# Kernel optimization log

Measured on AMD Instinct MI355X. Metric: run time of the kernel, lower is better.

## Reference

```python
import jax, jax.numpy as jnp
import numpy as np

L, H, P = 16384, 1024, 512
DT_MIN, DT_MAX = 1e-3, 1e-1


def setup_inputs() -> dict:
    key = jax.random.key(0)
    ks = jax.random.split(key, 9)
    input_sequence = jax.random.normal(ks[0], (L, H), dtype=jnp.float32)
    # HiPPO-like diagonal init: negative real parts, spread imaginary parts
    Lambda_re = -0.5 * jnp.ones((P,), dtype=jnp.float32)
    Lambda_im = jnp.pi * jnp.arange(P, dtype=jnp.float32)
    # B_tilde = Vinv @ B with lecun_normal B -> ~N(0, 1/H) entries
    B_re = jax.random.normal(ks[1], (P, H), dtype=jnp.float32) / np.float32(np.sqrt(H))
    B_im = jax.random.normal(ks[2], (P, H), dtype=jnp.float32) / np.float32(np.sqrt(H))
    # C_tilde = C @ V, lecun_normal scale ~1/sqrt(2P)
    C_re = jax.random.normal(ks[3], (H, P), dtype=jnp.float32) / np.float32(np.sqrt(2 * P))
    C_im = jax.random.normal(ks[4], (H, P), dtype=jnp.float32) / np.float32(np.sqrt(2 * P))
    D = jax.random.normal(ks[5], (H,), dtype=jnp.float32)
    # log_step ~ U[log(dt_min), log(dt_max)], shape (P, 1)
    u01 = jax.random.uniform(ks[6], (P, 1), dtype=jnp.float32)
    log_step = jnp.log(DT_MIN) + u01 * (jnp.log(DT_MAX) - jnp.log(DT_MIN))
    return {
        "input_sequence": input_sequence,
        "Lambda_re": Lambda_re, "Lambda_im": Lambda_im,
        "B_re": B_re, "B_im": B_im,
        "C_re": C_re, "C_im": C_im,
        "D": D, "log_step": log_step,
    }


def _binop(q_i, q_j):
    # diagonal linear recurrence combine: x_j = A_j * x_i + b_j
    A_i, b_i = q_i
    A_j, b_j = q_j
    return (A_j * A_i, A_j * b_i + b_j)


def reference(input_sequence, Lambda_re, Lambda_im, B_re, B_im, C_re, C_im, D, log_step):
    # step_rescale = 1.0, clip_eigs = False, conj_sym = True, zoh discretization
    step = jnp.exp(log_step[:, 0])                      # (P,)
    Lam = Lambda_re + 1j * Lambda_im                    # (P,) complex64
    Lambda_bar = jnp.exp(Lam * step)                    # (P,)
    B_tilde = B_re + 1j * B_im                          # (P, H)
    B_bar = ((Lambda_bar - 1.0) / Lam)[:, None] * B_tilde  # (P, H)

    # bf16-split complex matvec: Bu_t = B_bar @ u_t (u real) for all t at once
    Bre_bf = jnp.real(B_bar).astype(jnp.bfloat16)
    Bim_bf = jnp.imag(B_bar).astype(jnp.bfloat16)
    u_bf = input_sequence.astype(jnp.bfloat16)          # (L, H)
    Bu_re = jnp.einsum('ph,lh->lp', Bre_bf, u_bf).astype(jnp.float32)
    Bu_im = jnp.einsum('ph,lh->lp', Bim_bf, u_bf).astype(jnp.float32)
    Bu = Bu_re + 1j * Bu_im                             # (L, P) complex64

    Lambda_elems = Lambda_bar * jnp.ones((input_sequence.shape[0], Lambda_bar.shape[0]),
                                         dtype=Lambda_bar.dtype)  # (L, P)
    _, xs = jax.lax.associative_scan(_binop, (Lambda_elems, Bu))  # xs: (L, P) complex64

    # bf16-split complex matvec y = C_tilde @ x, keep real part only
    Cre_bf = C_re.astype(jnp.bfloat16)
    Cim_bf = C_im.astype(jnp.bfloat16)
    xre_bf = jnp.real(xs).astype(jnp.bfloat16)
    xim_bf = jnp.imag(xs).astype(jnp.bfloat16)
    rr = jnp.einsum('hp,lp->lh', Cre_bf, xre_bf)
    ii = jnp.einsum('hp,lp->lh', Cim_bf, xim_bf)
    y_real = (rr - ii).astype(jnp.float32)              # (L, H)
    ys = 2.0 * y_real                                   # conj_sym doubling

    # feedthrough
    return ys + D * input_sequence
```

## Files before the change

### kernel.cpp

```cpp
#include <hip/hip_runtime.h>
#include <stdint.h>
#include <stddef.h>

#define L_SEQ 16384
#define H_DIM 1024
#define P_DIM 512
#define N2P   1024
#define CHUNK 64
#define NCH   256

#define NB_U 8192
#define NB_B 256
#define NB_C 512
#define NB_T 2

typedef __bf16 bf16x8 __attribute__((ext_vector_type(8)));
typedef float  f32x4  __attribute__((ext_vector_type(4)));
typedef unsigned short u16x8 __attribute__((ext_vector_type(8)));
typedef unsigned int   u32x4 __attribute__((ext_vector_type(4)));

__device__ __forceinline__ unsigned short f2bf(float x) {
  unsigned int u = __float_as_uint(x);
  u += 0x7FFFu + ((u >> 16) & 1u);
  return (unsigned short)(u >> 16);
}
__device__ __forceinline__ float bf2f(unsigned short x) {
  return __uint_as_float((unsigned int)x << 16);
}

__global__ void k_pack_all(const float* __restrict__ U, unsigned short* __restrict__ Ub,
                           const float* __restrict__ Bre, const float* __restrict__ Bim,
                           unsigned short* __restrict__ Bp,
                           const float* __restrict__ Cre, const float* __restrict__ Cim,
                           unsigned short* __restrict__ Cp,
                           const float* __restrict__ Lre, const float* __restrict__ Lim,
                           const float* __restrict__ lstep,
                           float2* __restrict__ lam, float2* __restrict__ lamK) {
  int bid = blockIdx.x, tid = threadIdx.x;
  if (bid < NB_U) {
    size_t base = ((size_t)bid * 256 + tid) * 8;
    const float4* s = (const float4*)(U + base);
    float4 v0 = s[0], v1 = s[1];
    u16x8 o;
    o[0] = f2bf(v0.x); o[1] = f2bf(v0.y); o[2] = f2bf(v0.z); o[3] = f2bf(v0.w);
    o[4] = f2bf(v1.x); o[5] = f2bf(v1.y); o[6] = f2bf(v1.z); o[7] = f2bf(v1.w);
    *(u16x8*)(Ub + base) = o;
  } else if (bid < NB_U + NB_B) {
    int base = ((bid - NB_U) * 256 + tid) * 8;
    int p = base >> 10, h = base & 1023;
    float step = __expf(0.f) , sv, cv;
    step = expf(lstep[p]);
    float ar = Lre[p] * step, ai = Lim[p] * step;
    float er = expf(ar);
    sincosf(ai, &sv, &cv);
    float lr = er * cv, li = er * sv;
    float nr = lr - 1.0f, ni = li;
    float dr = Lre[p], di = Lim[p];
    float den = dr * dr + di * di;
    float cx = (nr * dr + ni * di) / den;
    float cy = (ni * dr - nr * di) / den;
    const float4* sre = (const float4*)(Bre + base);
    const float4* sim = (const float4*)(Bim + base);
    float4 r0 = sre[0], r1 = sre[1], i0 = sim[0], i1 = sim[1];
    u16x8 ore, oim;
    ore[0] = f2bf(cx * r0.x - cy * i0.x);  oim[0] = f2bf(cx * i0.x + cy * r0.x);
    ore[1] = f2bf(cx * r0.y - cy * i0.y);  oim[1] = f2bf(cx * i0.y + cy * r0.y);
    ore[2] = f2bf(cx * r0.z - cy * i0.z);  oim[2] = f2bf(cx * i0.z + cy * r0.z);
    ore[3] = f2bf(cx * r0.w - cy * i0.w);  oim[3] = f2bf(cx * i0.w + cy * r0.w);
    ore[4] = f2bf(cx * r1.x - cy * i1.x);  oim[4] = f2bf(cx * i1.x + cy * r1.x);
    ore[5] = f2bf(cx * r1.y - cy * i1.y);  oim[5] = f2bf(cx * i1.y + cy * r1.y);
    ore[6] = f2bf(cx * r1.z - cy * i1.z);  oim[6] = f2bf(cx * i1.z + cy * r1.z);
    ore[7] = f2bf(cx * r1.w - cy * i1.w);  oim[7] = f2bf(cx * i1.w + cy * r1.w);
    *(u16x8*)(Bp + (size_t)(2 * p) * H_DIM + h)     = ore;
    *(u16x8*)(Bp + (size_t)(2 * p + 1) * H_DIM + h) = oim;
  } else if (bid < NB_U + NB_B + NB_C) {
    int base = ((bid - NB_U - NB_B) * 256 + tid) * 8;
    int h = base >> 10, j0 = base & 1023;
    int p0 = j0 >> 1;
    float4 cr = *(const float4*)(Cre + (size_t)h * P_DIM + p0);
    float4 ci = *(const float4*)(Cim + (size_t)h * P_DIM + p0);
    u16x8 o;
    o[0] = f2bf(cr.x); o[1] = f2bf(-ci.x);
    o[2] = f2bf(cr.y); o[3] = f2bf(-ci.y);
    o[4] = f2bf(cr.z); o[5] = f2bf(-ci.z);
    o[6] = f2bf(cr.w); o[7] = f2bf(-ci.w);
    *(u16x8*)(Cp + base) = o;
  } else {
    int p = (bid - NB_U - NB_B - NB_C) * 256 + tid;
    if (p < P_DIM) {
      double step = exp((double)lstep[p]);
      double ar = (double)Lre[p] * step, ai = (double)Lim[p] * step;
      double er = exp(ar);
      lam[p] = make_float2((float)(er * cos(ai)), (float)(er * sin(ai)));
      double ka = (double)CHUNK * ai, kr = exp((double)CHUNK * ar);
      lamK[p] = make_float2((float)(kr * cos(ka)), (float)(kr * sin(ka)));
    }
  }
}

template <int OUT>
__global__ void gemm_bt(const unsigned short* __restrict__ A,
                        const unsigned short* __restrict__ B,
                        void* __restrict__ Cout,
                        const unsigned short* __restrict__ Ub,
                        const float* __restrict__ Dv) {
  const int K = 1024, N = 1024;
  __shared__ unsigned short sA[128 * 64];
  __shared__ unsigned short sB[128 * 64];
  const int tid = threadIdx.x;
  const int wave = tid >> 6, lane = tid & 63;
  const int quad = lane >> 4, l16 = lane & 15;
  const int m0 = blockIdx.x * 128, n0 = blockIdx.y * 128;
  const int wm = (wave & 1) * 64, wn = (wave >> 1) * 64;

  f32x4 acc[4][4] = {};

  for (int kt = 0; kt < K; kt += 64) {
    __syncthreads();
#pragma unroll
    for (int r = 0; r < 4; ++r) {
      int s = r * 256 + tid;
      int row = s >> 3;
      int j8 = (s & 7) ^ (row & 7);
      const unsigned short* ga = A + (size_t)(m0 + row) * K + kt + j8 * 8;
      const unsigned short* gb = B + (size_t)(n0 + row) * K + kt + j8 * 8;
      __builtin_amdgcn_global_load_lds(
          (const __attribute__((address_space(1))) unsigned int*)ga,
          (__attribute__((address_space(3))) unsigned int*)(sA + (r * 256 + wave * 64) * 8),
          16, 0, 0);
      __builtin_amdgcn_global_load_lds(
          (const __attribute__((address_space(1))) unsigned int*)gb,
          (__attribute__((address_space(3))) unsigned int*)(sB + (r * 256 + wave * 64) * 8),
          16, 0, 0);
    }
    __syncthreads();

#pragma unroll
    for (int h = 0; h < 2; ++h) {
      bf16x8 af[4], bfr[4];
#pragma unroll
      for (int i = 0; i < 4; ++i) {
        int ra = wm + i * 16 + l16;
        af[i] = *(const bf16x8*)(sA + ra * 64 + (((h << 2) + quad) ^ (ra & 7)) * 8);
      }
#pragma unroll
      for (int j = 0; j < 4; ++j) {
        int rb = wn + j * 16 + l16;
        bfr[j] = *(const bf16x8*)(sB + rb * 64 + (((h << 2) + quad) ^ (rb & 7)) * 8);
      }
#pragma unroll
      for (int i = 0; i < 4; ++i)
#pragma unroll
        for (int j = 0; j < 4; ++j)
          acc[i][j] = __builtin_amdgcn_mfma_f32_16x16x32_bf16(af[i], bfr[j], acc[i][j], 0, 0, 0);
    }
  }

#pragma unroll
  for (int i = 0; i < 4; ++i) {
#pragma unroll
    for (int j = 0; j < 4; ++j) {
      int col = n0 + wn + j * 16 + l16;
#pragma unroll
      for (int r = 0; r < 4; ++r) {
        int row = m0 + wm + i * 16 + quad * 4 + r;
        size_t o = (size_t)row * N + col;
        float v = acc[i][j][r];
        if (OUT) {
          float u = bf2f(Ub[o]);
          ((float*)Cout)[o] = 2.0f * v + Dv[col] * u;
        } else {
          ((unsigned short*)Cout)[o] = f2bf(v);
        }
      }
    }
  }
}

__global__ __launch_bounds__(256) void k_scanA(const unsigned short* __restrict__ Bu,
                                               const float2* __restrict__ lam,
                                               float2* __restrict__ csum) {
  __shared__ unsigned int tile[CHUNK * 256];
  const int bid = blockIdx.x;
  const int chunk = bid >> 1, half = bid & 1;
  const int tid = threadIdx.x, wave = tid >> 6, lane = tid & 63;
  const unsigned int* gbase =
      (const unsigned int*)(Bu + (size_t)chunk * CHUNK * N2P) + half * 256;
#pragma unroll
  for (int r = 0; r < 16; ++r) {
    int row = r * 4 + wave;
    __builtin_amdgcn_global_load_lds(
        (const __attribute__((address_space(1))) unsigned int*)
            (gbase + (size_t)row * (N2P / 2) + lane * 4),
        (__attribute__((address_space(3))) unsigned int*)(tile + row * 256),
        16, 0, 0);
  }
  __syncthreads();
  const int p = half * 256 + tid;
  const float2 l = lam[p];
  float xr = 0.f, xi = 0.f;
#pragma unroll 16
  for (int t = 0; t < CHUNK; ++t) {
    unsigned int v = tile[t * 256 + tid];
    float br = bf2f((unsigned short)(v & 0xffffu));
    float bi = bf2f((unsigned short)(v >> 16));
    float nr = fmaf(l.x, xr, fmaf(-l.y, xi, br));
    float ni = fmaf(l.x, xi, fmaf(l.y, xr, bi));
    xr = nr; xi = ni;
  }
  csum[(size_t)chunk * P_DIM + p] = make_float2(xr, xi);
}

__global__ __launch_bounds__(256) void k_scanC(const unsigned short* __restrict__ Bu,
                                               const float2* __restrict__ lam,
                                               const float2* __restrict__ lamK,
                                               const float2* __restrict__ csum,
                                               unsigned short* __restrict__ xs) {
  __shared__ unsigned int tile[CHUNK * 256];
  const int bid = blockIdx.x;
  const int chunk = bid >> 1, half = bid & 1;
  const int tid = threadIdx.x, wave = tid >> 6, lane = tid & 63;
  const unsigned int* gbase =
      (const unsigned int*)(Bu + (size_t)chunk * CHUNK * N2P) + half * 256;
#pragma unroll
  for (int r = 0; r < 16; ++r) {
    int row = r * 4 + wave;
    __builtin_amdgcn_global_load_lds(
        (const __attribute__((address_space(1))) unsigned int*)
            (gbase + (size_t)row * (N2P / 2) + lane * 4),
        (__attribute__((address_space(3))) unsigned int*)(tile + row * 256),
        16, 0, 0);
  }
  const int p = half * 256 + tid;
  const float2 l = lam[p];
  const float2 lk = lamK[p];
  float cr = 0.f, ci = 0.f;
#pragma unroll 4
  for (int j = 0; j < chunk; ++j) {
    float2 s = csum[(size_t)j * P_DIM + p];
    float nr = fmaf(lk.x, cr, fmaf(-lk.y, ci, s.x));
    float ni = fmaf(lk.x, ci, fmaf(lk.y, cr, s.y));
    cr = nr; ci = ni;
  }
  __syncthreads();
  float xr = cr, xi = ci;
#pragma unroll 16
  for (int t = 0; t < CHUNK; ++t) {
    unsigned int v = tile[t * 256 + tid];
    float br = bf2f((unsigned short)(v & 0xffffu));
    float bi = bf2f((unsigned short)(v >> 16));
    float nr = fmaf(l.x, xr, fmaf(-l.y, xi, br));
    float ni = fmaf(l.x, xi, fmaf(l.y, xr, bi));
    xr = nr; xi = ni;
    tile[t * 256 + tid] = (unsigned int)f2bf(xr) | ((unsigned int)f2bf(xi) << 16);
  }
  __syncthreads();
  unsigned int* obase = (unsigned int*)(xs + (size_t)chunk * CHUNK * N2P) + half * 256;
#pragma unroll
  for (int r = 0; r < 16; ++r) {
    int row = r * 4 + wave;
    *(u32x4*)(obase + (size_t)row * (N2P / 2) + lane * 4) =
        *(const u32x4*)(tile + row * 256 + lane * 4);
  }
}

extern "C" void kernel_launch(void* const* d_in, const int* in_sizes, int n_in,
                              void* d_out, int out_size, void* d_ws, size_t ws_size,
                              hipStream_t stream) {
  const float* U    = (const float*)d_in[0];
  const float* Lre  = (const float*)d_in[1];
  const float* Lim  = (const float*)d_in[2];
  const float* Bre  = (const float*)d_in[3];
  const float* Bim  = (const float*)d_in[4];
  const float* Cre  = (const float*)d_in[5];
  const float* Cim  = (const float*)d_in[6];
  const float* Dv   = (const float*)d_in[7];
  const float* lstp = (const float*)d_in[8];
  float* out = (float*)d_out;

  size_t off = 0;
  char* ws = (char*)d_ws;
  auto give = [&](size_t bytes) -> void* {
    void* p = ws + off;
    off += (bytes + 255) & ~(size_t)255;
    return p;
  };

  unsigned short* ubf  = (unsigned short*)give((size_t)L_SEQ * H_DIM * 2);
  unsigned short* Bp   = (unsigned short*)give((size_t)N2P * H_DIM * 2);
  unsigned short* Cp   = (unsigned short*)give((size_t)H_DIM * N2P * 2);
  unsigned short* Bu   = (unsigned short*)give((size_t)L_SEQ * N2P * 2);
  unsigned short* xs   = (unsigned short*)give((size_t)L_SEQ * N2P * 2);
  float2*         lam  = (float2*)give(P_DIM * sizeof(float2));
  float2*         lamK = (float2*)give(P_DIM * sizeof(float2));
  float2*         csum = (float2*)give((size_t)NCH * P_DIM * sizeof(float2));

  k_pack_all<<<NB_U + NB_B + NB_C + NB_T, 256, 0, stream>>>(
      U, ubf, Bre, Bim, Bp, Cre, Cim, Cp, Lre, Lim, lstp, lam, lamK);

  gemm_bt<0><<<dim3(L_SEQ / 128, N2P / 128), 256, 0, stream>>>(ubf, Bp, Bu, nullptr, nullptr);

  k_scanA<<<NCH * 2, 256, 0, stream>>>(Bu, lam, csum);
  k_scanC<<<NCH * 2, 256, 0, stream>>>(Bu, lam, lamK, csum, xs);

  gemm_bt<1><<<dim3(L_SEQ / 128, N2P / 128), 256, 0, stream>>>(xs, Cp, out, ubf, Dv);
}
```

Measured before the change: 262.9 us.

## Enlarge GEMM tiles to 256x256 with double-buffered async LDS loads

Both bf16 GEMMs now use 256x256 output tiles with 512 threads, where each wave computes a 128x64 sub-tile. The global-to-LDS loads are double-buffered: the next K-slice is prefetched while MFMAs run on the current one, with explicit vmcnt waits and barriers, and MFMA sections are raised in priority via s_setprio. This targets load latency and the low data reuse of the 128x128 tiles. The cost is 128KB of LDS per block and higher register use (32 accumulators), which can limit occupancy, and the grid shrinks to 256 blocks.

```diff
diff --git a/kernel.cpp b/kernel.cpp
--- a/kernel.cpp
+++ b/kernel.cpp
@@ -48,8 +48,8 @@
   } else if (bid < NB_U + NB_B) {
     int base = ((bid - NB_U) * 256 + tid) * 8;
     int p = base >> 10, h = base & 1023;
-    float step = __expf(0.f) , sv, cv;
-    step = expf(lstep[p]);
+    float sv, cv;
+    float step = expf(lstep[p]);
     float ar = Lre[p] * step, ai = Lim[p] * step;
     float er = expf(ar);
     sincosf(ai, &sv, &cv);
@@ -99,65 +99,91 @@
 }
 
 template <int OUT>
-__global__ void gemm_bt(const unsigned short* __restrict__ A,
+__global__ __launch_bounds__(512, 2) void gemm_bt(const unsigned short* __restrict__ A,
                         const unsigned short* __restrict__ B,
                         void* __restrict__ Cout,
                         const unsigned short* __restrict__ Ub,
                         const float* __restrict__ Dv) {
   const int K = 1024, N = 1024;
-  __shared__ unsigned short sA[128 * 64];
-  __shared__ unsigned short sB[128 * 64];
+  __shared__ unsigned short sA[2 * 256 * 64];
+  __shared__ unsigned short sB[2 * 256 * 64];
   const int tid = threadIdx.x;
-  const int wave = tid >> 6, lane = tid & 63;
+  const int w = tid >> 6, lane = tid & 63;
   const int quad = lane >> 4, l16 = lane & 15;
-  const int m0 = blockIdx.x * 128, n0 = blockIdx.y * 128;
-  const int wm = (wave & 1) * 64, wn = (wave >> 1) * 64;
-
-  f32x4 acc[4][4] = {};
-
-  for (int kt = 0; kt < K; kt += 64) {
-    __syncthreads();
+  const int m0 = blockIdx.x * 256, n0 = blockIdx.y * 256;
+  const int wm = (w & 1) * 128, wn = (w >> 1) * 64;
+
+  f32x4 acc[8][4] = {};
+
+  const unsigned short* ga[4];
+  const unsigned short* gb[4];
+#pragma unroll
+  for (int r = 0; r < 4; ++r) {
+    int s = r * 512 + tid;
+    int row = s >> 3;
+    int j8 = (s & 7) ^ (row & 7);
+    ga[r] = A + (size_t)(m0 + row) * K + j8 * 8;
+    gb[r] = B + (size_t)(n0 + row) * K + j8 * 8;
+  }
+
+  auto stage = [&](int buf, int kt) {
 #pragma unroll
     for (int r = 0; r < 4; ++r) {
-      int s = r * 256 + tid;
-      int row = s >> 3;
-      int j8 = (s & 7) ^ (row & 7);
-      const unsigned short* ga = A + (size_t)(m0 + row) * K + kt + j8 * 8;
-      const unsigned short* gb = B + (size_t)(n0 + row) * K + kt + j8 * 8;
       __builtin_amdgcn_global_load_lds(
-          (const __attribute__((address_space(1))) unsigned int*)ga,
-          (__attribute__((address_space(3))) unsigned int*)(sA + (r * 256 + wave * 64) * 8),
+          (const __attribute__((address_space(1))) unsigned int*)(ga[r] + kt),
+          (__attribute__((address_space(3))) unsigned int*)(sA + buf * 16384 + (r * 512 + w * 64) * 8),
           16, 0, 0);
       __builtin_amdgcn_global_load_lds(
-          (const __attribute__((address_space(1))) unsigned int*)gb,
-          (__attribute__((address_space(3))) unsigned int*)(sB + (r * 256 + wave * 64) * 8),
+          (const __attribute__((address_space(1))) unsigned int*)(gb[r] + kt),
+          (__attribute__((address_space(3))) unsigned int*)(sB + buf * 16384 + (r * 512 + w * 64) * 8),
           16, 0, 0);
     }
-    __syncthreads();
-
+  };
+
+  auto compute = [&](int buf) {
+    const unsigned short* sa = sA + buf * 16384;
+    const unsigned short* sb = sB + buf * 16384;
 #pragma unroll
     for (int h = 0; h < 2; ++h) {
-      bf16x8 af[4], bfr[4];
-#pragma unroll
-      for (int i = 0; i < 4; ++i) {
+      bf16x8 af[8], bfr[4];
+#pragma unroll
+      for (int i = 0; i < 8; ++i) {
         int ra = wm + i * 16 + l16;
-        af[i] = *(const bf16x8*)(sA + ra * 64 + (((h << 2) + quad) ^ (ra & 7)) * 8);
+        af[i] = *(const bf16x8*)(sa + ra * 64 + (((h << 2) + quad) ^ (ra & 7)) * 8);
       }
 #pragma unroll
       for (int j = 0; j < 4; ++j) {
         int rb = wn + j * 16 + l16;
-        bfr[j] = *(const bf16x8*)(sB + rb * 64 + (((h << 2) + quad) ^ (rb & 7)) * 8);
+        bfr[j] = *(const bf16x8*)(sb + rb * 64 + (((h << 2) + quad) ^ (rb & 7)) * 8);
       }
-#pragma unroll
-      for (int i = 0; i < 4; ++i)
+      __builtin_amdgcn_s_setprio(1);
+#pragma unroll
+      for (int i = 0; i < 8; ++i)
 #pragma unroll
         for (int j = 0; j < 4; ++j)
           acc[i][j] = __builtin_amdgcn_mfma_f32_16x16x32_bf16(af[i], bfr[j], acc[i][j], 0, 0, 0);
+      __builtin_amdgcn_s_setprio(0);
     }
-  }
-
-#pragma unroll
-  for (int i = 0; i < 4; ++i) {
+  };
+
+  stage(0, 0);
+  for (int t = 0; t < 15; ++t) {
+    stage((t + 1) & 1, (t + 1) * 64);
+    asm volatile("s_waitcnt vmcnt(8)" ::: "memory");
+    __builtin_amdgcn_s_barrier();
+    asm volatile("" ::: "memory");
+    compute(t & 1);
+    asm volatile("" ::: "memory");
+    __builtin_amdgcn_s_barrier();
+    asm volatile("" ::: "memory");
+  }
+  asm volatile("s_waitcnt vmcnt(0)" ::: "memory");
+  __builtin_amdgcn_s_barrier();
+  asm volatile("" ::: "memory");
+  compute(1);
+
+#pragma unroll
+  for (int i = 0; i < 8; ++i) {
 #pragma unroll
     for (int j = 0; j < 4; ++j) {
       int col = n0 + wn + j * 16 + l16;
@@ -298,10 +324,10 @@
   k_pack_all<<<NB_U + NB_B + NB_C + NB_T, 256, 0, stream>>>(
       U, ubf, Bre, Bim, Bp, Cre, Cim, Cp, Lre, Lim, lstp, lam, lamK);
 
-  gemm_bt<0><<<dim3(L_SEQ / 128, N2P / 128), 256, 0, stream>>>(ubf, Bp, Bu, nullptr, nullptr);
+  gemm_bt<0><<<dim3(L_SEQ / 256, N2P / 256), 512, 0, stream>>>(ubf, Bp, Bu, nullptr, nullptr);
 
   k_scanA<<<NCH * 2, 256, 0, stream>>>(Bu, lam, csum);
   k_scanC<<<NCH * 2, 256, 0, stream>>>(Bu, lam, lamK, csum, xs);
 
-  gemm_bt<1><<<dim3(L_SEQ / 128, N2P / 128), 256, 0, stream>>>(xs, Cp, out, ubf, Dv);
-}
+  gemm_bt<1><<<dim3(L_SEQ / 256, N2P / 256), 512, 0, stream>>>(xs, Cp, out, ubf, Dv);
+}
```

Result: no change. 259.4 us (-1.3%).

## Fuse two-pass chunked scan into one kernel with grid-wide atomic barrier

Applied to the files above, without the earlier changes.

Merges the chunk-summary kernel and the chunk-propagation kernel into a single launch. Blocks publish their chunk sums with atomic stores and then spin on a per-half counter until all chunks are done. Each block keeps its Bu tile in LDS across both phases, so Bu is no longer read from global memory twice and one kernel launch goes away. The spin barrier assumes all 512 blocks are resident at the same time, and it could deadlock if they are not.

```diff
diff --git a/kernel.cpp b/kernel.cpp
--- a/kernel.cpp
+++ b/kernel.cpp
@@ -35,7 +35,8 @@
                            unsigned short* __restrict__ Cp,
                            const float* __restrict__ Lre, const float* __restrict__ Lim,
                            const float* __restrict__ lstep,
-                           float2* __restrict__ lam, float2* __restrict__ lamK) {
+                           float2* __restrict__ lam, float2* __restrict__ lamK,
+                           int* __restrict__ cnt) {
   int bid = blockIdx.x, tid = threadIdx.x;
   if (bid < NB_U) {
     size_t base = ((size_t)bid * 256 + tid) * 8;
@@ -48,8 +49,8 @@
   } else if (bid < NB_U + NB_B) {
     int base = ((bid - NB_U) * 256 + tid) * 8;
     int p = base >> 10, h = base & 1023;
-    float step = __expf(0.f) , sv, cv;
-    step = expf(lstep[p]);
+    float sv, cv;
+    float step = expf(lstep[p]);
     float ar = Lre[p] * step, ai = Lim[p] * step;
     float er = expf(ar);
     sincosf(ai, &sv, &cv);
@@ -95,6 +96,10 @@
       double ka = (double)CHUNK * ai, kr = exp((double)CHUNK * ar);
       lamK[p] = make_float2((float)(kr * cos(ka)), (float)(kr * sin(ka)));
     }
+    if (p == 0) {
+      __hip_atomic_store(&cnt[0], 0, __ATOMIC_RELAXED, __HIP_MEMORY_SCOPE_AGENT);
+      __hip_atomic_store(&cnt[1], 0, __ATOMIC_RELAXED, __HIP_MEMORY_SCOPE_AGENT);
+    }
   }
 }
 
@@ -177,9 +182,12 @@
   }
 }
 
-__global__ __launch_bounds__(256) void k_scanA(const unsigned short* __restrict__ Bu,
-                                               const float2* __restrict__ lam,
-                                               float2* __restrict__ csum) {
+__global__ __launch_bounds__(256) void k_scan(const unsigned short* __restrict__ Bu,
+                                              const float2* __restrict__ lam,
+                                              const float2* __restrict__ lamK,
+                                              unsigned long long* __restrict__ csum,
+                                              int* __restrict__ cnt,
+                                              unsigned short* __restrict__ xs) {
   __shared__ unsigned int tile[CHUNK * 256];
   const int bid = blockIdx.x;
   const int chunk = bid >> 1, half = bid & 1;
@@ -198,51 +206,48 @@
   __syncthreads();
   const int p = half * 256 + tid;
   const float2 l = lam[p];
-  float xr = 0.f, xi = 0.f;
+
+  float sr = 0.f, si = 0.f;
 #pragma unroll 16
   for (int t = 0; t < CHUNK; ++t) {
     unsigned int v = tile[t * 256 + tid];
     float br = bf2f((unsigned short)(v & 0xffffu));
     float bi = bf2f((unsigned short)(v >> 16));
-    float nr = fmaf(l.x, xr, fmaf(-l.y, xi, br));
-    float ni = fmaf(l.x, xi, fmaf(l.y, xr, bi));
-    xr = nr; xi = ni;
-  }
-  csum[(size_t)chunk * P_DIM + p] = make_float2(xr, xi);
-}
-
-__global__ __launch_bounds__(256) void k_scanC(const unsigned short* __restrict__ Bu,
-                                               const float2* __restrict__ lam,
-                                               const float2* __restrict__ lamK,
-                                               const float2* __restrict__ csum,
-                                               unsigned short* __restrict__ xs) {
-  __shared__ unsigned int tile[CHUNK * 256];
-  const int bid = blockIdx.x;
-  const int chunk = bid >> 1, half = bid & 1;
-  const int tid = threadIdx.x, wave = tid >> 6, lane = tid & 63;
-  const unsigned int* gbase =
-      (const unsigned int*)(Bu + (size_t)chunk * CHUNK * N2P) + half * 256;
-#pragma unroll
-  for (int r = 0; r < 16; ++r) {
-    int row = r * 4 + wave;
-    __builtin_amdgcn_global_load_lds(
-        (const __attribute__((address_space(1))) unsigned int*)
-            (gbase + (size_t)row * (N2P / 2) + lane * 4),
-        (__attribute__((address_space(3))) unsigned int*)(tile + row * 256),
-        16, 0, 0);
-  }
-  const int p = half * 256 + tid;
-  const float2 l = lam[p];
-  const float2 lk = lamK[p];
+    float nr = fmaf(l.x, sr, fmaf(-l.y, si, br));
+    float ni = fmaf(l.x, si, fmaf(l.y, sr, bi));
+    sr = nr; si = ni;
+  }
+
+  union { float2 f; unsigned long long u; } pub;
+  pub.f = make_float2(sr, si);
+  __hip_atomic_store(&csum[(size_t)chunk * P_DIM + p], pub.u,
+                     __ATOMIC_RELAXED, __HIP_MEMORY_SCOPE_AGENT);
+  __syncthreads();
+  if (tid == 0) {
+    __threadfence();
+    __hip_atomic_fetch_add(&cnt[half], 1, __ATOMIC_RELEASE, __HIP_MEMORY_SCOPE_AGENT);
+  }
+
   float cr = 0.f, ci = 0.f;
+  if (chunk > 0) {
+    if (tid == 0) {
+      while (__hip_atomic_load(&cnt[half], __ATOMIC_ACQUIRE, __HIP_MEMORY_SCOPE_AGENT) < NCH) {
+        __builtin_amdgcn_s_sleep(2);
+      }
+    }
+    __syncthreads();
+    const float2 lk = lamK[p];
 #pragma unroll 4
-  for (int j = 0; j < chunk; ++j) {
-    float2 s = csum[(size_t)j * P_DIM + p];
-    float nr = fmaf(lk.x, cr, fmaf(-lk.y, ci, s.x));
-    float ni = fmaf(lk.x, ci, fmaf(lk.y, cr, s.y));
-    cr = nr; ci = ni;
-  }
-  __syncthreads();
+    for (int j = 0; j < chunk; ++j) {
+      union { float2 f; unsigned long long u; } s;
+      s.u = __hip_atomic_load(&csum[(size_t)j * P_DIM + p],
+                              __ATOMIC_RELAXED, __HIP_MEMORY_SCOPE_AGENT);
+      float nr = fmaf(lk.x, cr, fmaf(-lk.y, ci, s.f.x));
+      float ni = fmaf(lk.x, ci, fmaf(lk.y, cr, s.f.y));
+      cr = nr; ci = ni;
+    }
+  }
+
   float xr = cr, xi = ci;
 #pragma unroll 16
   for (int t = 0; t < CHUNK; ++t) {
@@ -293,15 +298,15 @@
   unsigned short* xs   = (unsigned short*)give((size_t)L_SEQ * N2P * 2);
   float2*         lam  = (float2*)give(P_DIM * sizeof(float2));
   float2*         lamK = (float2*)give(P_DIM * sizeof(float2));
-  float2*         csum = (float2*)give((size_t)NCH * P_DIM * sizeof(float2));
+  unsigned long long* csum = (unsigned long long*)give((size_t)NCH * P_DIM * 8);
+  int*            cnt  = (int*)give(256);
 
   k_pack_all<<<NB_U + NB_B + NB_C + NB_T, 256, 0, stream>>>(
-      U, ubf, Bre, Bim, Bp, Cre, Cim, Cp, Lre, Lim, lstp, lam, lamK);
+      U, ubf, Bre, Bim, Bp, Cre, Cim, Cp, Lre, Lim, lstp, lam, lamK, cnt);
 
   gemm_bt<0><<<dim3(L_SEQ / 128, N2P / 128), 256, 0, stream>>>(ubf, Bp, Bu, nullptr, nullptr);
 
-  k_scanA<<<NCH * 2, 256, 0, stream>>>(Bu, lam, csum);
-  k_scanC<<<NCH * 2, 256, 0, stream>>>(Bu, lam, lamK, csum, xs);
+  k_scan<<<NCH * 2, 256, 0, stream>>>(Bu, lam, lamK, csum, cnt, xs);
 
   gemm_bt<1><<<dim3(L_SEQ / 128, N2P / 128), 256, 0, stream>>>(xs, Cp, out, ubf, Dv);
 }
```

New measurement: 284.3 us. 8.1% more time.
